# Optimization experiments

Hardware: AMD Instinct MI355X
Metric: run time of the kernel (lower is better)

The kernel has to match this reference:

```python
import jax, jax.numpy as jnp
import numpy as np

B, C, H, W = 8, 512, 64, 64
M = C // 8  # query/key channels
EPS = 1e-6

def setup_inputs() -> dict:
    key = jax.random.key(0)
    ks = jax.random.split(key, 8)
    s_in = 0.02
    return {
        "x": jax.random.normal(ks[0], (B, C, H, W), dtype=jnp.float32),
        "Wq": jax.random.normal(ks[1], (M, C), dtype=jnp.float32) * s_in,
        "bq": jnp.zeros((M,), dtype=jnp.float32),
        "Wk": jax.random.normal(ks[2], (M, C), dtype=jnp.float32) * s_in,
        "bk": jnp.zeros((M,), dtype=jnp.float32),
        "Wv": jax.random.normal(ks[3], (C, C), dtype=jnp.float32) * s_in,
        "bv": jnp.zeros((C,), dtype=jnp.float32),
        "gamma": jax.random.uniform(ks[4], (1,), dtype=jnp.float32) * 0.5,
    }

def _l2_norm(t):
    # normalize over channel dim (axis=-2), per position; matches torch.norm(p=2, dim=-2)
    return t / jnp.linalg.norm(t, axis=-2, keepdims=True)

def reference(x, Wq, bq, Wk, bk, Wv, bv, gamma):
    b, c, h, w = x.shape
    n = h * w
    xf = x.reshape(b, c, n)                               # [b,c,n]
    # 1x1 convs as channel GEMMs
    Q = jnp.einsum('mc,bcn->bmn', Wq, xf) + bq[None, :, None]   # [b,m,n]
    K = jnp.einsum('mc,bcn->bmn', Wk, xf) + bk[None, :, None]   # [b,m,n]
    V = jnp.einsum('dc,bcn->bdn', Wv, xf) + bv[None, :, None]   # [b,c,n]
    Qn = _l2_norm(Q).transpose(0, 2, 1)                   # [b,n,m]
    Kn = _l2_norm(K)                                      # [b,m,n]
    # denominator: 1 / (N + Q . sum_n(K))
    tailor = 1.0 / (n + jnp.einsum('bnm,bm->bn', Qn, Kn.sum(axis=-1) + EPS))  # [b,n]
    value_sum = V.sum(axis=-1)                            # [b,c]
    matrix = jnp.einsum('bmn,bcn->bmc', Kn, V)            # [b,m,c] (O(N) contraction)
    matrix_sum = value_sum[:, :, None] + jnp.einsum('bnm,bmc->bcn', Qn, matrix)  # [b,c,n]
    weight_value = matrix_sum * tailor[:, None, :]        # [b,c,n]
    return x + gamma * weight_value.reshape(b, c, h, w)
```

## Files before the change

### kernel.cpp

```cpp
#include <hip/hip_runtime.h>
#include <hip/hip_bf16.h>

constexpr int B = 8;
constexpr int C = 512;
constexpr int M = 64;
constexpr int N = 4096;
constexpr float EPS = 1e-6f;
constexpr int NTS = 8;
constexpr int LDP = 72;
constexpr int LDPF = 68;

typedef __attribute__((ext_vector_type(8))) short short8v;
typedef __attribute__((ext_vector_type(4))) short short4v;
typedef __attribute__((ext_vector_type(4))) float f32x4;

__device__ __forceinline__ short f2b(float f) {
  union { __hip_bfloat16 h; short s; } u;
  u.h = __float2bfloat16(f);
  return u.s;
}
__device__ __forceinline__ float b2f(short s) {
  union { __hip_bfloat16 h; short s2; } u;
  u.s2 = s;
  return __bfloat162float(u.h);
}

__global__ __launch_bounds__(256) void prep_kernel(
    const float* __restrict__ Wq, const float* __restrict__ Wk,
    const float* __restrict__ Wv, short* __restrict__ Wq_bf,
    short* __restrict__ Wk_bf, short* __restrict__ Wv_bf,
    float* __restrict__ Ksum, float* __restrict__ xsum) {
  const int id = blockIdx.x * 256 + threadIdx.x;
  const int stride = gridDim.x * 256;
  for (int i = id; i < C * M / 4; i += stride) {
    const float4 a = reinterpret_cast<const float4*>(Wq)[i];
    const float4 b = reinterpret_cast<const float4*>(Wk)[i];
    short4v sa = {f2b(a.x), f2b(a.y), f2b(a.z), f2b(a.w)};
    short4v sb = {f2b(b.x), f2b(b.y), f2b(b.z), f2b(b.w)};
    reinterpret_cast<short4v*>(Wq_bf)[i] = sa;
    reinterpret_cast<short4v*>(Wk_bf)[i] = sb;
  }
  for (int i = id; i < C * C / 4; i += stride) {
    const float4 a = reinterpret_cast<const float4*>(Wv)[i];
    short4v sa = {f2b(a.x), f2b(a.y), f2b(a.z), f2b(a.w)};
    reinterpret_cast<short4v*>(Wv_bf)[i] = sa;
  }
  for (int i = id; i < B * M + B * C; i += stride) {
    if (i < B * M) Ksum[i] = 0.f;
    else xsum[i - B * M] = 0.f;
  }
}

__global__ __launch_bounds__(256) void qk_kernel(
    const float* __restrict__ x, const short* __restrict__ Wq_bf,
    const float* __restrict__ bq, const short* __restrict__ Wk_bf,
    const float* __restrict__ bk, short* __restrict__ QnT,
    short* __restrict__ KnB, float* __restrict__ Ksum) {
  __shared__ short aq[64 * LDP];
  __shared__ short ak[64 * LDP];
  __shared__ short bx[64 * LDP];
  __shared__ float colred[2][4][64];
  __shared__ float rsq[2][64];
  const int t = threadIdx.x;
  const int n0 = blockIdx.x * 64;
  const int b = blockIdx.y;
  const int w = t >> 6, l = t & 63, l15 = l & 15, kg = l >> 4;
  f32x4 accQ[4], accK[4];
#pragma unroll
  for (int i = 0; i < 4; ++i) { accQ[i] = f32x4{0.f, 0.f, 0.f, 0.f}; accK[i] = f32x4{0.f, 0.f, 0.f, 0.f}; }

  for (int c0 = 0; c0 < C; c0 += 64) {
    __syncthreads();
    {
      const int m = t >> 2, ko = (t & 3) * 16;
      *reinterpret_cast<short8v*>(&aq[m * LDP + ko]) =
          *reinterpret_cast<const short8v*>(&Wq_bf[m * C + c0 + ko]);
      *reinterpret_cast<short8v*>(&aq[m * LDP + ko + 8]) =
          *reinterpret_cast<const short8v*>(&Wq_bf[m * C + c0 + ko + 8]);
      *reinterpret_cast<short8v*>(&ak[m * LDP + ko]) =
          *reinterpret_cast<const short8v*>(&Wk_bf[m * C + c0 + ko]);
      *reinterpret_cast<short8v*>(&ak[m * LDP + ko + 8]) =
          *reinterpret_cast<const short8v*>(&Wk_bf[m * C + c0 + ko + 8]);
      const int cr = t & 63, ng = t >> 6;
      const float* xg = x + ((size_t)b * C + c0 + cr) * N + n0 + ng * 16;
      float vv[16];
#pragma unroll
      for (int i = 0; i < 4; ++i) {
        const float4 v = *reinterpret_cast<const float4*>(xg + 4 * i);
        vv[4 * i + 0] = v.x; vv[4 * i + 1] = v.y; vv[4 * i + 2] = v.z; vv[4 * i + 3] = v.w;
      }
#pragma unroll
      for (int i = 0; i < 16; ++i) bx[(ng * 16 + i) * LDP + cr] = f2b(vv[i]);
    }
    __syncthreads();
#pragma unroll
    for (int ks = 0; ks < 2; ++ks) {
      const short8v afq = *reinterpret_cast<const short8v*>(&aq[(w * 16 + l15) * LDP + ks * 32 + kg * 8]);
      const short8v afk = *reinterpret_cast<const short8v*>(&ak[(w * 16 + l15) * LDP + ks * 32 + kg * 8]);
#pragma unroll
      for (int tc = 0; tc < 4; ++tc) {
        const short8v bf = *reinterpret_cast<const short8v*>(&bx[(tc * 16 + l15) * LDP + ks * 32 + kg * 8]);
        accQ[tc] = __builtin_amdgcn_mfma_f32_16x16x32_bf16(afq, bf, accQ[tc], 0, 0, 0);
        accK[tc] = __builtin_amdgcn_mfma_f32_16x16x32_bf16(afk, bf, accK[tc], 0, 0, 0);
      }
    }
  }
  {
    const float4 q4 = *reinterpret_cast<const float4*>(&bq[w * 16 + kg * 4]);
    const float4 k4 = *reinterpret_cast<const float4*>(&bk[w * 16 + kg * 4]);
    const float bqa[4] = {q4.x, q4.y, q4.z, q4.w};
    const float bka[4] = {k4.x, k4.y, k4.z, k4.w};
#pragma unroll
    for (int tc = 0; tc < 4; ++tc)
#pragma unroll
      for (int r = 0; r < 4; ++r) { accQ[tc][r] += bqa[r]; accK[tc][r] += bka[r]; }
  }
#pragma unroll
  for (int tc = 0; tc < 4; ++tc) {
    float vq = accQ[tc][0] * accQ[tc][0] + accQ[tc][1] * accQ[tc][1] +
               accQ[tc][2] * accQ[tc][2] + accQ[tc][3] * accQ[tc][3];
    float vk = accK[tc][0] * accK[tc][0] + accK[tc][1] * accK[tc][1] +
               accK[tc][2] * accK[tc][2] + accK[tc][3] * accK[tc][3];
    vq += __shfl_xor(vq, 16, 64); vq += __shfl_xor(vq, 32, 64);
    vk += __shfl_xor(vk, 16, 64); vk += __shfl_xor(vk, 32, 64);
    if (l < 16) { colred[0][w][tc * 16 + l] = vq; colred[1][w][tc * 16 + l] = vk; }
  }
  __syncthreads();
  if (t < 128) {
    const int which = t >> 6, n = t & 63;
    const float s = colred[which][0][n] + colred[which][1][n] +
                    colred[which][2][n] + colred[which][3][n];
    rsq[which][n] = 1.0f / sqrtf(s);
  }
  __syncthreads();
  float ksr[4] = {0.f, 0.f, 0.f, 0.f};
#pragma unroll
  for (int tc = 0; tc < 4; ++tc) {
    const float rq = rsq[0][tc * 16 + l15], rk = rsq[1][tc * 16 + l15];
#pragma unroll
    for (int r = 0; r < 4; ++r) { accQ[tc][r] *= rq; accK[tc][r] *= rk; ksr[r] += accK[tc][r]; }
  }
#pragma unroll
  for (int r = 0; r < 4; ++r) {
    float s = ksr[r];
    s += __shfl_xor(s, 1, 64); s += __shfl_xor(s, 2, 64);
    s += __shfl_xor(s, 4, 64); s += __shfl_xor(s, 8, 64);
    if (l15 == 0) atomicAdd(&Ksum[b * M + w * 16 + kg * 4 + r], s);
  }
#pragma unroll
  for (int tc = 0; tc < 4; ++tc) {
    short4v q4 = {f2b(accQ[tc][0]), f2b(accQ[tc][1]), f2b(accQ[tc][2]), f2b(accQ[tc][3])};
    *reinterpret_cast<short4v*>(&aq[(tc * 16 + l15) * LDP + w * 16 + kg * 4]) = q4;
#pragma unroll
    for (int r = 0; r < 4; ++r)
      ak[(w * 16 + kg * 4 + r) * LDP + tc * 16 + l15] = f2b(accK[tc][r]);
  }
  __syncthreads();
  {
    const int r = t >> 2, ko = (t & 3) * 16;
    short* qg = QnT + ((size_t)b * N + n0 + r) * M + ko;
    *reinterpret_cast<short8v*>(qg) = *reinterpret_cast<const short8v*>(&aq[r * LDP + ko]);
    *reinterpret_cast<short8v*>(qg + 8) = *reinterpret_cast<const short8v*>(&aq[r * LDP + ko + 8]);
    short* kg2 = KnB + ((size_t)b * M + r) * N + n0 + ko;
    *reinterpret_cast<short8v*>(kg2) = *reinterpret_cast<const short8v*>(&ak[r * LDP + ko]);
    *reinterpret_cast<short8v*>(kg2 + 8) = *reinterpret_cast<const short8v*>(&ak[r * LDP + ko + 8]);
  }
}

__global__ __launch_bounds__(256) void s_kernel(
    const float* __restrict__ x, const short* __restrict__ KnB,
    float* __restrict__ Spart, float* __restrict__ xsum) {
  __shared__ short sm[2 * 64 * LDP];
  __shared__ float red[256];
  short* ka = sm;
  short* xb = sm + 64 * LDP;
  const int t = threadIdx.x;
  const int c0 = blockIdx.x * 64;
  const int nt = blockIdx.y;
  const int b = blockIdx.z;
  const int w = t >> 6, l = t & 63, l15 = l & 15, kg = l >> 4;
  f32x4 acc[4];
#pragma unroll
  for (int i = 0; i < 4; ++i) acc[i] = f32x4{0.f, 0.f, 0.f, 0.f};
  float xacc = 0.f;
  for (int it = 0; it < (N / NTS) / 64; ++it) {
    const int nk = nt * (N / NTS) + it * 64;
    __syncthreads();
    {
      const int r = t >> 2, ko = (t & 3) * 16;
      *reinterpret_cast<short8v*>(&ka[r * LDP + ko]) =
          *reinterpret_cast<const short8v*>(&KnB[((size_t)b * M + r) * N + nk + ko]);
      *reinterpret_cast<short8v*>(&ka[r * LDP + ko + 8]) =
          *reinterpret_cast<const short8v*>(&KnB[((size_t)b * M + r) * N + nk + ko + 8]);
      const float* xg = x + ((size_t)b * C + c0 + r) * N + nk + ko;
      float vv[16];
#pragma unroll
      for (int i = 0; i < 4; ++i) {
        const float4 v = *reinterpret_cast<const float4*>(xg + 4 * i);
        vv[4 * i] = v.x; vv[4 * i + 1] = v.y; vv[4 * i + 2] = v.z; vv[4 * i + 3] = v.w;
        xacc += v.x + v.y + v.z + v.w;
      }
      short tmp[16];
#pragma unroll
      for (int i = 0; i < 16; ++i) tmp[i] = f2b(vv[i]);
      *reinterpret_cast<short8v*>(&xb[r * LDP + ko]) = *reinterpret_cast<const short8v*>(&tmp[0]);
      *reinterpret_cast<short8v*>(&xb[r * LDP + ko + 8]) = *reinterpret_cast<const short8v*>(&tmp[8]);
    }
    __syncthreads();
#pragma unroll
    for (int ks = 0; ks < 2; ++ks) {
      const short8v af = *reinterpret_cast<const short8v*>(&ka[(w * 16 + l15) * LDP + ks * 32 + kg * 8]);
#pragma unroll
      for (int tc = 0; tc < 4; ++tc) {
        const short8v bf = *reinterpret_cast<const short8v*>(&xb[(tc * 16 + l15) * LDP + ks * 32 + kg * 8]);
        acc[tc] = __builtin_amdgcn_mfma_f32_16x16x32_bf16(af, bf, acc[tc], 0, 0, 0);
      }
    }
  }
  red[t] = xacc;
  __syncthreads();
  if (t < 64)
    atomicAdd(&xsum[b * C + c0 + t], red[4 * t] + red[4 * t + 1] + red[4 * t + 2] + red[4 * t + 3]);
  float* bo = reinterpret_cast<float*>(sm);
#pragma unroll
  for (int tc = 0; tc < 4; ++tc)
#pragma unroll
    for (int r = 0; r < 4; ++r)
      bo[(w * 16 + kg * 4 + r) * LDPF + tc * 16 + l15] = acc[tc][r];
  __syncthreads();
  {
    const int m = t >> 2, ko = (t & 3) * 16;
    float* gp = Spart + (((size_t)nt * B + b) * M + m) * C + c0 + ko;
#pragma unroll
    for (int i = 0; i < 4; ++i)
      *reinterpret_cast<float4*>(gp + 4 * i) = *reinterpret_cast<const float4*>(&bo[m * LDPF + ko + 4 * i]);
  }
}

__global__ __launch_bounds__(256) void sreduce_kernel(const float* __restrict__ Spart,
                                                      short* __restrict__ S_bf) {
  const int i4 = blockIdx.x * 256 + threadIdx.x;
  const size_t stride = (size_t)B * M * C;
  const float* p = Spart + (size_t)i4 * 4;
  float s0 = 0.f, s1 = 0.f, s2 = 0.f, s3 = 0.f;
#pragma unroll
  for (int nt = 0; nt < NTS; ++nt) {
    const float4 v = *reinterpret_cast<const float4*>(p + nt * stride);
    s0 += v.x; s1 += v.y; s2 += v.z; s3 += v.w;
  }
  short4v o = {f2b(s0), f2b(s1), f2b(s2), f2b(s3)};
  *reinterpret_cast<short4v*>(&S_bf[(size_t)i4 * 4]) = o;
}

__global__ __launch_bounds__(256) void matm_kernel(
    const short* __restrict__ Wv_bf, const float* __restrict__ bv,
    const short* __restrict__ S_bf, const float* __restrict__ xsum,
    const float* __restrict__ Ksum, short* __restrict__ matMT,
    float* __restrict__ vsum) {
  __shared__ short wa[64 * LDP];
  __shared__ short sb[64 * LDP];
  __shared__ float xs[64];
  const int t = threadIdx.x;
  const int c0 = blockIdx.x * 64;
  const int b = blockIdx.y;
  const int w = t >> 6, l = t & 63, l15 = l & 15, kg = l >> 4;
  f32x4 acc[4];
#pragma unroll
  for (int i = 0; i < 4; ++i) acc[i] = f32x4{0.f, 0.f, 0.f, 0.f};
  float vacc = 0.f;
  for (int k0 = 0; k0 < C; k0 += 64) {
    __syncthreads();
    {
      const int r = t >> 2, ko = (t & 3) * 16;
      *reinterpret_cast<short8v*>(&wa[r * LDP + ko]) =
          *reinterpret_cast<const short8v*>(&Wv_bf[(size_t)(c0 + r) * C + k0 + ko]);
      *reinterpret_cast<short8v*>(&wa[r * LDP + ko + 8]) =
          *reinterpret_cast<const short8v*>(&Wv_bf[(size_t)(c0 + r) * C + k0 + ko + 8]);
      *reinterpret_cast<short8v*>(&sb[r * LDP + ko]) =
          *reinterpret_cast<const short8v*>(&S_bf[((size_t)b * M + r) * C + k0 + ko]);
      *reinterpret_cast<short8v*>(&sb[r * LDP + ko + 8]) =
          *reinterpret_cast<const short8v*>(&S_bf[((size_t)b * M + r) * C + k0 + ko + 8]);
    }
    if (t < 64) xs[t] = xsum[b * C + k0 + t];
    __syncthreads();
#pragma unroll
    for (int ks = 0; ks < 2; ++ks) {
      const short8v af = *reinterpret_cast<const short8v*>(&wa[(w * 16 + l15) * LDP + ks * 32 + kg * 8]);
#pragma unroll
      for (int tc = 0; tc < 4; ++tc) {
        const short8v bf = *reinterpret_cast<const short8v*>(&sb[(tc * 16 + l15) * LDP + ks * 32 + kg * 8]);
        acc[tc] = __builtin_amdgcn_mfma_f32_16x16x32_bf16(af, bf, acc[tc], 0, 0, 0);
      }
    }
    if (t < 64) {
      float v = 0.f;
#pragma unroll 8
      for (int kk = 0; kk < 64; ++kk) v = fmaf(b2f(wa[t * LDP + kk]), xs[kk], v);
      vacc += v;
    }
  }
  __syncthreads();
  {
    const float4 b4 = *reinterpret_cast<const float4*>(&bv[c0 + w * 16 + kg * 4]);
    const float bva[4] = {b4.x, b4.y, b4.z, b4.w};
#pragma unroll
    for (int tc = 0; tc < 4; ++tc) {
      const float ksm = Ksum[b * M + tc * 16 + l15];
#pragma unroll
      for (int r = 0; r < 4; ++r)
        wa[(w * 16 + kg * 4 + r) * LDP + tc * 16 + l15] = f2b(acc[tc][r] + bva[r] * ksm);
    }
  }
  __syncthreads();
  {
    const int r = t >> 2, ko = (t & 3) * 16;
    short* gp = matMT + ((size_t)b * C + c0 + r) * M + ko;
    *reinterpret_cast<short8v*>(gp) = *reinterpret_cast<const short8v*>(&wa[r * LDP + ko]);
    *reinterpret_cast<short8v*>(gp + 8) = *reinterpret_cast<const short8v*>(&wa[r * LDP + ko + 8]);
  }
  if (t < 64) vsum[b * C + c0 + t] = vacc + 4096.0f * bv[c0 + t];
}

__global__ __launch_bounds__(256) void final_kernel(
    const float* __restrict__ x, const short* __restrict__ QnT,
    const float* __restrict__ Ksum, const short* __restrict__ matMT,
    const float* __restrict__ vsum, const float* __restrict__ gamma,
    float* __restrict__ out) {
  __shared__ short qb[64 * LDP];
  __shared__ short ab[64 * LDP];
  __shared__ float bo[64 * LDPF];
  __shared__ float ke[64];
  __shared__ float tl[64];
  __shared__ float red2[256];
  const int t = threadIdx.x;
  const int n0 = blockIdx.x * 64;
  const int b = blockIdx.y;
  const int w = t >> 6, l = t & 63, l15 = l & 15, kg = l >> 4;
  {
    const int r = t >> 2, ko = (t & 3) * 16;
    *reinterpret_cast<short8v*>(&qb[r * LDP + ko]) =
        *reinterpret_cast<const short8v*>(&QnT[((size_t)b * N + n0 + r) * M + ko]);
    *reinterpret_cast<short8v*>(&qb[r * LDP + ko + 8]) =
        *reinterpret_cast<const short8v*>(&QnT[((size_t)b * N + n0 + r) * M + ko + 8]);
  }
  if (t < 64) ke[t] = Ksum[b * M + t] + EPS;
  __syncthreads();
  {
    const int n = t & 63, mq = t >> 6;
    float d = 0.f;
#pragma unroll
    for (int j = 0; j < 16; ++j) d = fmaf(b2f(qb[n * LDP + mq * 16 + j]), ke[mq * 16 + j], d);
    red2[t] = d;
  }
  __syncthreads();
  if (t < 64)
    tl[t] = 1.0f / (4096.0f + red2[t] + red2[64 + t] + red2[128 + t] + red2[192 + t]);
  const float g = gamma[0];
  for (int c0 = 0; c0 < C; c0 += 64) {
    __syncthreads();
    {
      const int r = t >> 2, ko = (t & 3) * 16;
      *reinterpret_cast<short8v*>(&ab[r * LDP + ko]) =
          *reinterpret_cast<const short8v*>(&matMT[((size_t)b * C + c0 + r) * M + ko]);
      *reinterpret_cast<short8v*>(&ab[r * LDP + ko + 8]) =
          *reinterpret_cast<const short8v*>(&matMT[((size_t)b * C + c0 + r) * M + ko + 8]);
    }
    __syncthreads();
    f32x4 acc[4];
#pragma unroll
    for (int i = 0; i < 4; ++i) acc[i] = f32x4{0.f, 0.f, 0.f, 0.f};
#pragma unroll
    for (int ks = 0; ks < 2; ++ks) {
      const short8v af = *reinterpret_cast<const short8v*>(&ab[(w * 16 + l15) * LDP + ks * 32 + kg * 8]);
#pragma unroll
      for (int tc = 0; tc < 4; ++tc) {
        const short8v bf = *reinterpret_cast<const short8v*>(&qb[(tc * 16 + l15) * LDP + ks * 32 + kg * 8]);
        acc[tc] = __builtin_amdgcn_mfma_f32_16x16x32_bf16(af, bf, acc[tc], 0, 0, 0);
      }
    }
#pragma unroll
    for (int tc = 0; tc < 4; ++tc)
#pragma unroll
      for (int r = 0; r < 4; ++r)
        bo[(w * 16 + kg * 4 + r) * LDPF + tc * 16 + l15] = acc[tc][r];
    __syncthreads();
    {
      const int r = t >> 2, ko = (t & 3) * 16;
      const int c = c0 + r;
      const float vs = vsum[b * C + c];
      const size_t off = ((size_t)b * C + c) * N + n0 + ko;
#pragma unroll
      for (int i = 0; i < 4; ++i) {
        const float4 xv = *reinterpret_cast<const float4*>(&x[off + 4 * i]);
        const float4 dv = *reinterpret_cast<const float4*>(&bo[r * LDPF + ko + 4 * i]);
        const float4 tv = *reinterpret_cast<const float4*>(&tl[ko + 4 * i]);
        float4 o;
        o.x = xv.x + g * tv.x * (vs + dv.x);
        o.y = xv.y + g * tv.y * (vs + dv.y);
        o.z = xv.z + g * tv.z * (vs + dv.z);
        o.w = xv.w + g * tv.w * (vs + dv.w);
        *reinterpret_cast<float4*>(&out[off + 4 * i]) = o;
      }
    }
  }
}

extern "C" void kernel_launch(void* const* d_in, const int* in_sizes, int n_in,
                              void* d_out, int out_size, void* d_ws, size_t ws_size,
                              hipStream_t stream) {
  (void)in_sizes; (void)n_in; (void)out_size; (void)ws_size;
  const float* x = (const float*)d_in[0];
  const float* Wq = (const float*)d_in[1];
  const float* bq = (const float*)d_in[2];
  const float* Wk = (const float*)d_in[3];
  const float* bk = (const float*)d_in[4];
  const float* Wv = (const float*)d_in[5];
  const float* bv = (const float*)d_in[6];
  const float* gamma = (const float*)d_in[7];
  float* out = (float*)d_out;

  char* wp = (char*)d_ws;
  short* Wq_bf = (short*)wp;            wp += (size_t)C * M * 2;
  short* Wk_bf = (short*)wp;            wp += (size_t)C * M * 2;
  short* Wv_bf = (short*)wp;            wp += (size_t)C * C * 2;
  short* KnB   = (short*)wp;            wp += (size_t)B * M * N * 2;
  short* QnT   = (short*)wp;            wp += (size_t)B * N * M * 2;
  short* S_bf  = (short*)wp;            wp += (size_t)B * M * C * 2;
  short* matMT = (short*)wp;            wp += (size_t)B * C * M * 2;
  float* Spart = (float*)wp;            wp += (size_t)NTS * B * M * C * 4;
  float* Ksum  = (float*)wp;            wp += (size_t)B * M * 4;
  float* xsum  = (float*)wp;            wp += (size_t)B * C * 4;
  float* vsum  = (float*)wp;            wp += (size_t)B * C * 4;

  prep_kernel<<<256, 256, 0, stream>>>(Wq, Wk, Wv, Wq_bf, Wk_bf, Wv_bf, Ksum, xsum);
  qk_kernel<<<dim3(N / 64, B), 256, 0, stream>>>(x, Wq_bf, bq, Wk_bf, bk, QnT, KnB, Ksum);
  s_kernel<<<dim3(C / 64, NTS, B), 256, 0, stream>>>(x, KnB, Spart, xsum);
  sreduce_kernel<<<B * M * C / 4 / 256, 256, 0, stream>>>(Spart, S_bf);
  matm_kernel<<<dim3(C / 64, B), 256, 0, stream>>>(Wv_bf, bv, S_bf, xsum, Ksum, matMT, vsum);
  final_kernel<<<dim3(N / 64, B), 256, 0, stream>>>(x, QnT, Ksum, matMT, vsum, gamma, out);
}
```

Before: 195.1 us.

## Prefetch tiles into registers, fold split-N reduction into matm, split final grid

Measured after the change: 207.2 us. 6.2% more time.

```diff
diff --git a/kernel.cpp b/kernel.cpp
--- a/kernel.cpp
+++ b/kernel.cpp
@@ -6,7 +6,7 @@
 constexpr int M = 64;
 constexpr int N = 4096;
 constexpr float EPS = 1e-6f;
-constexpr int NTS = 8;
+constexpr int NTS = 16;
 constexpr int LDP = 72;
 constexpr int LDPF = 68;
 
@@ -65,34 +65,47 @@
   const int n0 = blockIdx.x * 64;
   const int b = blockIdx.y;
   const int w = t >> 6, l = t & 63, l15 = l & 15, kg = l >> 4;
+  const int sr = t >> 2, sko = (t & 3) * 16;
+  const int cr = t & 63, ng = t >> 6;
   f32x4 accQ[4], accK[4];
 #pragma unroll
   for (int i = 0; i < 4; ++i) { accQ[i] = f32x4{0.f, 0.f, 0.f, 0.f}; accK[i] = f32x4{0.f, 0.f, 0.f, 0.f}; }
 
+  short8v wq0, wq1, wk0, wk1;
+  float4 xr[4];
+  {
+    wq0 = *reinterpret_cast<const short8v*>(&Wq_bf[sr * C + sko]);
+    wq1 = *reinterpret_cast<const short8v*>(&Wq_bf[sr * C + sko + 8]);
+    wk0 = *reinterpret_cast<const short8v*>(&Wk_bf[sr * C + sko]);
+    wk1 = *reinterpret_cast<const short8v*>(&Wk_bf[sr * C + sko + 8]);
+    const float* xg = x + ((size_t)b * C + cr) * N + n0 + ng * 16;
+#pragma unroll
+    for (int i = 0; i < 4; ++i) xr[i] = *reinterpret_cast<const float4*>(xg + 4 * i);
+  }
   for (int c0 = 0; c0 < C; c0 += 64) {
     __syncthreads();
-    {
-      const int m = t >> 2, ko = (t & 3) * 16;
-      *reinterpret_cast<short8v*>(&aq[m * LDP + ko]) =
-          *reinterpret_cast<const short8v*>(&Wq_bf[m * C + c0 + ko]);
-      *reinterpret_cast<short8v*>(&aq[m * LDP + ko + 8]) =
-          *reinterpret_cast<const short8v*>(&Wq_bf[m * C + c0 + ko + 8]);
-      *reinterpret_cast<short8v*>(&ak[m * LDP + ko]) =
-          *reinterpret_cast<const short8v*>(&Wk_bf[m * C + c0 + ko]);
-      *reinterpret_cast<short8v*>(&ak[m * LDP + ko + 8]) =
-          *reinterpret_cast<const short8v*>(&Wk_bf[m * C + c0 + ko + 8]);
-      const int cr = t & 63, ng = t >> 6;
-      const float* xg = x + ((size_t)b * C + c0 + cr) * N + n0 + ng * 16;
-      float vv[16];
-#pragma unroll
-      for (int i = 0; i < 4; ++i) {
-        const float4 v = *reinterpret_cast<const float4*>(xg + 4 * i);
-        vv[4 * i + 0] = v.x; vv[4 * i + 1] = v.y; vv[4 * i + 2] = v.z; vv[4 * i + 3] = v.w;
-      }
-#pragma unroll
-      for (int i = 0; i < 16; ++i) bx[(ng * 16 + i) * LDP + cr] = f2b(vv[i]);
-    }
-    __syncthreads();
+    *reinterpret_cast<short8v*>(&aq[sr * LDP + sko]) = wq0;
+    *reinterpret_cast<short8v*>(&aq[sr * LDP + sko + 8]) = wq1;
+    *reinterpret_cast<short8v*>(&ak[sr * LDP + sko]) = wk0;
+    *reinterpret_cast<short8v*>(&ak[sr * LDP + sko + 8]) = wk1;
+#pragma unroll
+    for (int i = 0; i < 4; ++i) {
+      bx[(ng * 16 + 4 * i + 0) * LDP + cr] = f2b(xr[i].x);
+      bx[(ng * 16 + 4 * i + 1) * LDP + cr] = f2b(xr[i].y);
+      bx[(ng * 16 + 4 * i + 2) * LDP + cr] = f2b(xr[i].z);
+      bx[(ng * 16 + 4 * i + 3) * LDP + cr] = f2b(xr[i].w);
+    }
+    __syncthreads();
+    if (c0 + 64 < C) {
+      const int c1 = c0 + 64;
+      wq0 = *reinterpret_cast<const short8v*>(&Wq_bf[sr * C + c1 + sko]);
+      wq1 = *reinterpret_cast<const short8v*>(&Wq_bf[sr * C + c1 + sko + 8]);
+      wk0 = *reinterpret_cast<const short8v*>(&Wk_bf[sr * C + c1 + sko]);
+      wk1 = *reinterpret_cast<const short8v*>(&Wk_bf[sr * C + c1 + sko + 8]);
+      const float* xg = x + ((size_t)b * C + c1 + cr) * N + n0 + ng * 16;
+#pragma unroll
+      for (int i = 0; i < 4; ++i) xr[i] = *reinterpret_cast<const float4*>(xg + 4 * i);
+    }
 #pragma unroll
     for (int ks = 0; ks < 2; ++ks) {
       const short8v afq = *reinterpret_cast<const short8v*>(&aq[(w * 16 + l15) * LDP + ks * 32 + kg * 8]);
@@ -157,19 +170,18 @@
   }
   __syncthreads();
   {
-    const int r = t >> 2, ko = (t & 3) * 16;
-    short* qg = QnT + ((size_t)b * N + n0 + r) * M + ko;
-    *reinterpret_cast<short8v*>(qg) = *reinterpret_cast<const short8v*>(&aq[r * LDP + ko]);
-    *reinterpret_cast<short8v*>(qg + 8) = *reinterpret_cast<const short8v*>(&aq[r * LDP + ko + 8]);
-    short* kg2 = KnB + ((size_t)b * M + r) * N + n0 + ko;
-    *reinterpret_cast<short8v*>(kg2) = *reinterpret_cast<const short8v*>(&ak[r * LDP + ko]);
-    *reinterpret_cast<short8v*>(kg2 + 8) = *reinterpret_cast<const short8v*>(&ak[r * LDP + ko + 8]);
+    short* qg = QnT + ((size_t)b * N + n0 + sr) * M + sko;
+    *reinterpret_cast<short8v*>(qg) = *reinterpret_cast<const short8v*>(&aq[sr * LDP + sko]);
+    *reinterpret_cast<short8v*>(qg + 8) = *reinterpret_cast<const short8v*>(&aq[sr * LDP + sko + 8]);
+    short* kg2 = KnB + ((size_t)b * M + sr) * N + n0 + sko;
+    *reinterpret_cast<short8v*>(kg2) = *reinterpret_cast<const short8v*>(&ak[sr * LDP + sko]);
+    *reinterpret_cast<short8v*>(kg2 + 8) = *reinterpret_cast<const short8v*>(&ak[sr * LDP + sko + 8]);
   }
 }
 
 __global__ __launch_bounds__(256) void s_kernel(
     const float* __restrict__ x, const short* __restrict__ KnB,
-    float* __restrict__ Spart, float* __restrict__ xsum) {
+    short* __restrict__ Spart, float* __restrict__ xsum) {
   __shared__ short sm[2 * 64 * LDP];
   __shared__ float red[256];
   short* ka = sm;
@@ -179,34 +191,46 @@
   const int nt = blockIdx.y;
   const int b = blockIdx.z;
   const int w = t >> 6, l = t & 63, l15 = l & 15, kg = l >> 4;
+  const int sr = t >> 2, sko = (t & 3) * 16;
   f32x4 acc[4];
 #pragma unroll
   for (int i = 0; i < 4; ++i) acc[i] = f32x4{0.f, 0.f, 0.f, 0.f};
   float xacc = 0.f;
-  for (int it = 0; it < (N / NTS) / 64; ++it) {
-    const int nk = nt * (N / NTS) + it * 64;
-    __syncthreads();
-    {
-      const int r = t >> 2, ko = (t & 3) * 16;
-      *reinterpret_cast<short8v*>(&ka[r * LDP + ko]) =
-          *reinterpret_cast<const short8v*>(&KnB[((size_t)b * M + r) * N + nk + ko]);
-      *reinterpret_cast<short8v*>(&ka[r * LDP + ko + 8]) =
-          *reinterpret_cast<const short8v*>(&KnB[((size_t)b * M + r) * N + nk + ko + 8]);
-      const float* xg = x + ((size_t)b * C + c0 + r) * N + nk + ko;
-      float vv[16];
-#pragma unroll
-      for (int i = 0; i < 4; ++i) {
-        const float4 v = *reinterpret_cast<const float4*>(xg + 4 * i);
-        vv[4 * i] = v.x; vv[4 * i + 1] = v.y; vv[4 * i + 2] = v.z; vv[4 * i + 3] = v.w;
-        xacc += v.x + v.y + v.z + v.w;
-      }
-      short tmp[16];
-#pragma unroll
-      for (int i = 0; i < 16; ++i) tmp[i] = f2b(vv[i]);
-      *reinterpret_cast<short8v*>(&xb[r * LDP + ko]) = *reinterpret_cast<const short8v*>(&tmp[0]);
-      *reinterpret_cast<short8v*>(&xb[r * LDP + ko + 8]) = *reinterpret_cast<const short8v*>(&tmp[8]);
-    }
-    __syncthreads();
+  constexpr int ITERS = N / NTS / 64;
+  const int nbase = nt * (N / NTS);
+  short8v k0r, k1r;
+  float4 xr[4];
+  {
+    const short* kp = &KnB[((size_t)b * M + sr) * N + nbase + sko];
+    k0r = *reinterpret_cast<const short8v*>(kp);
+    k1r = *reinterpret_cast<const short8v*>(kp + 8);
+    const float* xg = x + ((size_t)b * C + c0 + sr) * N + nbase + sko;
+#pragma unroll
+    for (int i = 0; i < 4; ++i) xr[i] = *reinterpret_cast<const float4*>(xg + 4 * i);
+  }
+  for (int it = 0; it < ITERS; ++it) {
+    __syncthreads();
+    *reinterpret_cast<short8v*>(&ka[sr * LDP + sko]) = k0r;
+    *reinterpret_cast<short8v*>(&ka[sr * LDP + sko + 8]) = k1r;
+    short tmp[16];
+#pragma unroll
+    for (int i = 0; i < 4; ++i) {
+      tmp[4 * i + 0] = f2b(xr[i].x); tmp[4 * i + 1] = f2b(xr[i].y);
+      tmp[4 * i + 2] = f2b(xr[i].z); tmp[4 * i + 3] = f2b(xr[i].w);
+      xacc += xr[i].x + xr[i].y + xr[i].z + xr[i].w;
+    }
+    *reinterpret_cast<short8v*>(&xb[sr * LDP + sko]) = *reinterpret_cast<const short8v*>(&tmp[0]);
+    *reinterpret_cast<short8v*>(&xb[sr * LDP + sko + 8]) = *reinterpret_cast<const short8v*>(&tmp[8]);
+    __syncthreads();
+    if (it + 1 < ITERS) {
+      const int nk = nbase + (it + 1) * 64;
+      const short* kp = &KnB[((size_t)b * M + sr) * N + nk + sko];
+      k0r = *reinterpret_cast<const short8v*>(kp);
+      k1r = *reinterpret_cast<const short8v*>(kp + 8);
+      const float* xg = x + ((size_t)b * C + c0 + sr) * N + nk + sko;
+#pragma unroll
+      for (int i = 0; i < 4; ++i) xr[i] = *reinterpret_cast<const float4*>(xg + 4 * i);
+    }
 #pragma unroll
     for (int ks = 0; ks < 2; ++ks) {
       const short8v af = *reinterpret_cast<const short8v*>(&ka[(w * 16 + l15) * LDP + ks * 32 + kg * 8]);
@@ -221,40 +245,22 @@
   __syncthreads();
   if (t < 64)
     atomicAdd(&xsum[b * C + c0 + t], red[4 * t] + red[4 * t + 1] + red[4 * t + 2] + red[4 * t + 3]);
-  float* bo = reinterpret_cast<float*>(sm);
 #pragma unroll
   for (int tc = 0; tc < 4; ++tc)
 #pragma unroll
     for (int r = 0; r < 4; ++r)
-      bo[(w * 16 + kg * 4 + r) * LDPF + tc * 16 + l15] = acc[tc][r];
-  __syncthreads();
-  {
-    const int m = t >> 2, ko = (t & 3) * 16;
-    float* gp = Spart + (((size_t)nt * B + b) * M + m) * C + c0 + ko;
-#pragma unroll
-    for (int i = 0; i < 4; ++i)
-      *reinterpret_cast<float4*>(gp + 4 * i) = *reinterpret_cast<const float4*>(&bo[m * LDPF + ko + 4 * i]);
-  }
-}
-
-__global__ __launch_bounds__(256) void sreduce_kernel(const float* __restrict__ Spart,
-                                                      short* __restrict__ S_bf) {
-  const int i4 = blockIdx.x * 256 + threadIdx.x;
-  const size_t stride = (size_t)B * M * C;
-  const float* p = Spart + (size_t)i4 * 4;
-  float s0 = 0.f, s1 = 0.f, s2 = 0.f, s3 = 0.f;
-#pragma unroll
-  for (int nt = 0; nt < NTS; ++nt) {
-    const float4 v = *reinterpret_cast<const float4*>(p + nt * stride);
-    s0 += v.x; s1 += v.y; s2 += v.z; s3 += v.w;
-  }
-  short4v o = {f2b(s0), f2b(s1), f2b(s2), f2b(s3)};
-  *reinterpret_cast<short4v*>(&S_bf[(size_t)i4 * 4]) = o;
+      sm[(w * 16 + kg * 4 + r) * LDP + tc * 16 + l15] = f2b(acc[tc][r]);
+  __syncthreads();
+  {
+    short* gp = Spart + (((size_t)nt * B + b) * M + sr) * C + c0 + sko;
+    *reinterpret_cast<short8v*>(gp) = *reinterpret_cast<const short8v*>(&sm[sr * LDP + sko]);
+    *reinterpret_cast<short8v*>(gp + 8) = *reinterpret_cast<const short8v*>(&sm[sr * LDP + sko + 8]);
+  }
 }
 
 __global__ __launch_bounds__(256) void matm_kernel(
     const short* __restrict__ Wv_bf, const float* __restrict__ bv,
-    const short* __restrict__ S_bf, const float* __restrict__ xsum,
+    const short* __restrict__ Spart, const float* __restrict__ xsum,
     const float* __restrict__ Ksum, short* __restrict__ matMT,
     float* __restrict__ vsum) {
   __shared__ short wa[64 * LDP];
@@ -264,22 +270,34 @@
   const int c0 = blockIdx.x * 64;
   const int b = blockIdx.y;
   const int w = t >> 6, l = t & 63, l15 = l & 15, kg = l >> 4;
+  const int sr = t >> 2, sko = (t & 3) * 16;
   f32x4 acc[4];
 #pragma unroll
   for (int i = 0; i < 4; ++i) acc[i] = f32x4{0.f, 0.f, 0.f, 0.f};
   float vacc = 0.f;
   for (int k0 = 0; k0 < C; k0 += 64) {
     __syncthreads();
+    *reinterpret_cast<short8v*>(&wa[sr * LDP + sko]) =
+        *reinterpret_cast<const short8v*>(&Wv_bf[(size_t)(c0 + sr) * C + k0 + sko]);
+    *reinterpret_cast<short8v*>(&wa[sr * LDP + sko + 8]) =
+        *reinterpret_cast<const short8v*>(&Wv_bf[(size_t)(c0 + sr) * C + k0 + sko + 8]);
     {
-      const int r = t >> 2, ko = (t & 3) * 16;
-      *reinterpret_cast<short8v*>(&wa[r * LDP + ko]) =
-          *reinterpret_cast<const short8v*>(&Wv_bf[(size_t)(c0 + r) * C + k0 + ko]);
-      *reinterpret_cast<short8v*>(&wa[r * LDP + ko + 8]) =
-          *reinterpret_cast<const short8v*>(&Wv_bf[(size_t)(c0 + r) * C + k0 + ko + 8]);
-      *reinterpret_cast<short8v*>(&sb[r * LDP + ko]) =
-          *reinterpret_cast<const short8v*>(&S_bf[((size_t)b * M + r) * C + k0 + ko]);
-      *reinterpret_cast<short8v*>(&sb[r * LDP + ko + 8]) =
-          *reinterpret_cast<const short8v*>(&S_bf[((size_t)b * M + r) * C + k0 + ko + 8]);
+      float sacc[16];
+#pragma unroll
+      for (int j = 0; j < 16; ++j) sacc[j] = 0.f;
+#pragma unroll 4
+      for (int nt2 = 0; nt2 < NTS; ++nt2) {
+        const short* sp = Spart + (((size_t)nt2 * B + b) * M + sr) * C + k0 + sko;
+        const short8v p0 = *reinterpret_cast<const short8v*>(sp);
+        const short8v p1 = *reinterpret_cast<const short8v*>(sp + 8);
+#pragma unroll
+        for (int j = 0; j < 8; ++j) { sacc[j] += b2f(p0[j]); sacc[8 + j] += b2f(p1[j]); }
+      }
+      short tmp[16];
+#pragma unroll
+      for (int j = 0; j < 16; ++j) tmp[j] = f2b(sacc[j]);
+      *reinterpret_cast<short8v*>(&sb[sr * LDP + sko]) = *reinterpret_cast<const short8v*>(&tmp[0]);
+      *reinterpret_cast<short8v*>(&sb[sr * LDP + sko + 8]) = *reinterpret_cast<const short8v*>(&tmp[8]);
     }
     if (t < 64) xs[t] = xsum[b * C + k0 + t];
     __syncthreads();
@@ -313,10 +331,9 @@
   }
   __syncthreads();
   {
-    const int r = t >> 2, ko = (t & 3) * 16;
-    short* gp = matMT + ((size_t)b * C + c0 + r) * M + ko;
-    *reinterpret_cast<short8v*>(gp) = *reinterpret_cast<const short8v*>(&wa[r * LDP + ko]);
-    *reinterpret_cast<short8v*>(gp + 8) = *reinterpret_cast<const short8v*>(&wa[r * LDP + ko + 8]);
+    short* gp = matMT + ((size_t)b * C + c0 + sr) * M + sko;
+    *reinterpret_cast<short8v*>(gp) = *reinterpret_cast<const short8v*>(&wa[sr * LDP + sko]);
+    *reinterpret_cast<short8v*>(gp + 8) = *reinterpret_cast<const short8v*>(&wa[sr * LDP + sko + 8]);
   }
   if (t < 64) vsum[b * C + c0 + t] = vacc + 4096.0f * bv[c0 + t];
 }
@@ -334,14 +351,14 @@
   __shared__ float red2[256];
   const int t = threadIdx.x;
   const int n0 = blockIdx.x * 64;
-  const int b = blockIdx.y;
+  const int cy = blockIdx.y;
+  const int b = blockIdx.z;
   const int w = t >> 6, l = t & 63, l15 = l & 15, kg = l >> 4;
-  {
-    const int r = t >> 2, ko = (t & 3) * 16;
-    *reinterpret_cast<short8v*>(&qb[r * LDP + ko]) =
-        *reinterpret_cast<const short8v*>(&QnT[((size_t)b * N + n0 + r) * M + ko]);
-    *reinterpret_cast<short8v*>(&qb[r * LDP + ko + 8]) =
-        *reinterpret_cast<const short8v*>(&QnT[((size_t)b * N + n0 + r) * M + ko + 8]);
+  const int sr = t >> 2, sko = (t & 3) * 16;
+  {
+    const short* qg = &QnT[((size_t)b * N + n0 + sr) * M + sko];
+    *reinterpret_cast<short8v*>(&qb[sr * LDP + sko]) = *reinterpret_cast<const short8v*>(qg);
+    *reinterpret_cast<short8v*>(&qb[sr * LDP + sko + 8]) = *reinterpret_cast<const short8v*>(qg + 8);
   }
   if (t < 64) ke[t] = Ksum[b * M + t] + EPS;
   __syncthreads();
@@ -356,16 +373,29 @@
   if (t < 64)
     tl[t] = 1.0f / (4096.0f + red2[t] + red2[64 + t] + red2[128 + t] + red2[192 + t]);
   const float g = gamma[0];
-  for (int c0 = 0; c0 < C; c0 += 64) {
-    __syncthreads();
+  short8v ar0, ar1;
+  {
+    const short* mp = &matMT[((size_t)b * C + cy * 256 + sr) * M + sko];
+    ar0 = *reinterpret_cast<const short8v*>(mp);
+    ar1 = *reinterpret_cast<const short8v*>(mp + 8);
+  }
+  for (int cc = 0; cc < 4; ++cc) {
+    const int c0 = cy * 256 + cc * 64;
+    __syncthreads();
+    *reinterpret_cast<short8v*>(&ab[sr * LDP + sko]) = ar0;
+    *reinterpret_cast<short8v*>(&ab[sr * LDP + sko + 8]) = ar1;
+    __syncthreads();
+    if (cc < 3) {
+      const short* mp = &matMT[((size_t)b * C + c0 + 64 + sr) * M + sko];
+      ar0 = *reinterpret_cast<const short8v*>(mp);
+      ar1 = *reinterpret_cast<const short8v*>(mp + 8);
+    }
+    float4 xr[4];
     {
-      const int r = t >> 2, ko = (t & 3) * 16;
-      *reinterpret_cast<short8v*>(&ab[r * LDP + ko]) =
-          *reinterpret_cast<const short8v*>(&matMT[((size_t)b * C + c0 + r) * M + ko]);
-      *reinterpret_cast<short8v*>(&ab[r * LDP + ko + 8]) =
-          *reinterpret_cast<const short8v*>(&matMT[((size_t)b * C + c0 + r) * M + ko + 8]);
-    }
-    __syncthreads();
+      const float* xp = &x[((size_t)b * C + c0 + sr) * N + n0 + sko];
+#pragma unroll
+      for (int i = 0; i < 4; ++i) xr[i] = *reinterpret_cast<const float4*>(xp + 4 * i);
+    }
     f32x4 acc[4];
 #pragma unroll
     for (int i = 0; i < 4; ++i) acc[i] = f32x4{0.f, 0.f, 0.f, 0.f};
@@ -385,20 +415,18 @@
         bo[(w * 16 + kg * 4 + r) * LDPF + tc * 16 + l15] = acc[tc][r];
     __syncthreads();
     {
-      const int r = t >> 2, ko = (t & 3) * 16;
-      const int c = c0 + r;
+      const int c = c0 + sr;
       const float vs = vsum[b * C + c];
-      const size_t off = ((size_t)b * C + c) * N + n0 + ko;
+      const size_t off = ((size_t)b * C + c) * N + n0 + sko;
 #pragma unroll
       for (int i = 0; i < 4; ++i) {
-        const float4 xv = *reinterpret_cast<const float4*>(&x[off + 4 * i]);
-        const float4 dv = *reinterpret_cast<const float4*>(&bo[r * LDPF + ko + 4 * i]);
-        const float4 tv = *reinterpret_cast<const float4*>(&tl[ko + 4 * i]);
+        const float4 dv = *reinterpret_cast<const float4*>(&bo[sr * LDPF + sko + 4 * i]);
+        const float4 tv = *reinterpret_cast<const float4*>(&tl[sko + 4 * i]);
         float4 o;
-        o.x = xv.x + g * tv.x * (vs + dv.x);
-        o.y = xv.y + g * tv.y * (vs + dv.y);
-        o.z = xv.z + g * tv.z * (vs + dv.z);
-        o.w = xv.w + g * tv.w * (vs + dv.w);
+        o.x = xr[i].x + g * tv.x * (vs + dv.x);
+        o.y = xr[i].y + g * tv.y * (vs + dv.y);
+        o.z = xr[i].z + g * tv.z * (vs + dv.z);
+        o.w = xr[i].w + g * tv.w * (vs + dv.w);
         *reinterpret_cast<float4*>(&out[off + 4 * i]) = o;
       }
     }
@@ -420,22 +448,20 @@
   float* out = (float*)d_out;
 
   char* wp = (char*)d_ws;
-  short* Wq_bf = (short*)wp;            wp += (size_t)C * M * 2;
-  short* Wk_bf = (short*)wp;            wp += (size_t)C * M * 2;
-  short* Wv_bf = (short*)wp;            wp += (size_t)C * C * 2;
-  short* KnB   = (short*)wp;            wp += (size_t)B * M * N * 2;
-  short* QnT   = (short*)wp;            wp += (size_t)B * N * M * 2;
-  short* S_bf  = (short*)wp;            wp += (size_t)B * M * C * 2;
-  short* matMT = (short*)wp;            wp += (size_t)B * C * M * 2;
-  float* Spart = (float*)wp;            wp += (size_t)NTS * B * M * C * 4;
-  float* Ksum  = (float*)wp;            wp += (size_t)B * M * 4;
-  float* xsum  = (float*)wp;            wp += (size_t)B * C * 4;
-  float* vsum  = (float*)wp;            wp += (size_t)B * C * 4;
+  short* Wq_bf = (short*)wp;  wp += (size_t)C * M * 2;
+  short* Wk_bf = (short*)wp;  wp += (size_t)C * M * 2;
+  short* Wv_bf = (short*)wp;  wp += (size_t)C * C * 2;
+  short* KnB   = (short*)wp;  wp += (size_t)B * M * N * 2;
+  short* QnT   = (short*)wp;  wp += (size_t)B * N * M * 2;
+  short* matMT = (short*)wp;  wp += (size_t)B * C * M * 2;
+  short* Spart = (short*)wp;  wp += (size_t)NTS * B * M * C * 2;
+  float* Ksum  = (float*)wp;  wp += (size_t)B * M * 4;
+  float* xsum  = (float*)wp;  wp += (size_t)B * C * 4;
+  float* vsum  = (float*)wp;  wp += (size_t)B * C * 4;
 
   prep_kernel<<<256, 256, 0, stream>>>(Wq, Wk, Wv, Wq_bf, Wk_bf, Wv_bf, Ksum, xsum);
   qk_kernel<<<dim3(N / 64, B), 256, 0, stream>>>(x, Wq_bf, bq, Wk_bf, bk, QnT, KnB, Ksum);
   s_kernel<<<dim3(C / 64, NTS, B), 256, 0, stream>>>(x, KnB, Spart, xsum);
-  sreduce_kernel<<<B * M * C / 4 / 256, 256, 0, stream>>>(Spart, S_bf);
-  matm_kernel<<<dim3(C / 64, B), 256, 0, stream>>>(Wv_bf, bv, S_bf, xsum, Ksum, matMT, vsum);
-  final_kernel<<<dim3(N / 64, B), 256, 0, stream>>>(x, QnT, Ksum, matMT, vsum, gamma, out);
-}
+  matm_kernel<<<dim3(C / 64, B), 256, 0, stream>>>(Wv_bf, bv, Spart, xsum, Ksum, matMT, vsum);
+  final_kernel<<<dim3(N / 64, 2, B), 256, 0, stream>>>(x, QnT, Ksum, matMT, vsum, gamma, out);
+}
```
